# Performance work log

Measured on AMD Instinct MI355X. Metric: run time of the kernel, lower is better.

The kernel has to match this reference:

```python
import jax, jax.numpy as jnp
import numpy as np

# ---- static config (mirrors Anchors.__init__ defaults) ----
STRIDES = [8, 16, 32, 64]
SIZES = [32, 64, 128, 256]
RATIOS = np.array([0.5, 1.0, 2.0])
SCALES = np.array([2 ** 0, 2 ** (1.0 / 3.0), 2 ** (2.0 / 3.0)])
FG_IOU, BG_IOU = 0.5, 0.4
VAR_XY, VAR_WH = 0.1, 0.2


def _anchor_wh(box_size, ratios, scales):
    # Faithful to AnchorLayer.generate_anchors
    a = box_size * np.tile(scales, (2, len(ratios))).T  # [K, 2]
    areas = a[:, 0] * a[:, 1]
    rr = np.repeat(ratios, len(scales))
    w = np.sqrt(areas * rr)
    h = w / rr
    return np.stack([w, h], axis=1).astype(np.float32)  # [K, 2]


def _level_anchors(H, W, stride, box_size):
    wh = _anchor_wh(box_size, RATIOS, SCALES)            # [K, 2]
    K = wh.shape[0]
    xs = (np.arange(W, dtype=np.float32) + 0.5) * stride
    ys = (np.arange(H, dtype=np.float32) + 0.5) * stride
    gx, gy = np.meshgrid(xs, ys)                         # [H, W] each
    grid = np.stack([gx, gy], axis=-1)[:, :, None, :]    # [H, W, 1, 2]
    grid = np.broadcast_to(grid, (H, W, K, 2))
    whb = np.broadcast_to(wh[None, None], (H, W, K, 2))
    return np.concatenate([grid, whb], axis=-1).reshape(-1, 4)  # xywh


def make_anchors(feature_shapes):
    levels = [_level_anchors(h, w, s, bs)
              for (h, w), s, bs in zip(feature_shapes, STRIDES, SIZES)]
    anchors = jnp.asarray(np.concatenate(levels, axis=0))  # [A, 4] xywh
    half = anchors[:, 2:] * 0.5
    anchors_xyxy = jnp.concatenate([anchors[:, :2] - half,
                                    anchors[:, :2] + half], axis=-1)
    return anchors, anchors_xyxy


def batch_box_iou(a_xyxy, g_xyxy):
    # a_xyxy: [A, 4], g_xyxy: [B, M, 4] -> [B, A, M]
    lt = jnp.maximum(a_xyxy[None, :, None, :2], g_xyxy[:, None, :, :2])
    rb = jnp.minimum(a_xyxy[None, :, None, 2:], g_xyxy[:, None, :, 2:])
    wh = jnp.clip(rb - lt, 0.0)
    inter = wh[..., 0] * wh[..., 1]
    area_a = (a_xyxy[:, 2] - a_xyxy[:, 0]) * (a_xyxy[:, 3] - a_xyxy[:, 1])
    area_g = (g_xyxy[..., 2] - g_xyxy[..., 0]) * (g_xyxy[..., 3] - g_xyxy[..., 1])
    return inter / (area_a[None, :, None] + area_g[:, None, :] - inter)


def bbox_to_deltas(boxes_xyxy, anchors_xywh):
    # boxes_xyxy: [B, A, 4], anchors_xywh: [A, 4]
    axy, awh = anchors_xywh[:, :2], anchors_xywh[:, 2:]
    cxcy = (boxes_xyxy[..., :2] + boxes_xyxy[..., 2:]) * 0.5
    txy = (cxcy - axy) / (awh * VAR_XY)
    twh = jnp.log((boxes_xyxy[..., 2:] - boxes_xyxy[..., :2]) / awh) / VAR_WH
    return jnp.concatenate([txy, twh], axis=-1)


def setup_inputs() -> dict:
    key = jax.random.key(0)
    ks = jax.random.split(key, 8)
    B, M = 16, 64
    f3 = jax.random.normal(ks[0], (B, 64, 64, 64), dtype=jnp.float32)
    f4 = jax.random.normal(ks[1], (B, 64, 32, 32), dtype=jnp.float32)
    f5 = jax.random.normal(ks[2], (B, 64, 16, 16), dtype=jnp.float32)
    f6 = jax.random.normal(ks[3], (B, 64, 8, 8), dtype=jnp.float32)
    # valid gt boxes in a 512x512 image, xyxy format
    cxy = jax.random.uniform(ks[4], (B, M, 2), minval=60.0, maxval=452.0)
    wh = jax.random.uniform(ks[5], (B, M, 2), minval=10.0, maxval=110.0)
    gt_boxes = jnp.concatenate([cxy - wh * 0.5, cxy + wh * 0.5], axis=-1)
    gt_labels = jax.random.randint(ks[6], (B, M), 1, 21, dtype=jnp.int64)
    return {"f3": f3, "f4": f4, "f5": f5, "f6": f6,
            "gt_boxes": gt_boxes, "gt_labels": gt_labels}


def reference(f3, f4, f5, f6, gt_boxes, gt_labels):
    feats = [f3, f4, f5, f6]
    shapes = [f.shape[-2:] for f in feats]
    anchors, anchors_xyxy = make_anchors(shapes)      # [A,4], [A,4]

    ious = batch_box_iou(anchors_xyxy, gt_boxes)      # [B, A, M]
    best_iou = ious.max(axis=-1)                      # [B, A]
    best_idx = ious.argmax(axis=-1)                   # [B, A]

    mask_bg = best_iou < BG_IOU
    mask_ign = (best_iou > BG_IOU) & (best_iou < FG_IOU)

    labels = jnp.take_along_axis(gt_labels, best_idx, axis=1)     # [B, A]
    labels = jnp.where(mask_ign, -1, labels)
    labels = jnp.where(mask_bg, 0, labels)

    boxes = jnp.take_along_axis(gt_boxes, best_idx[..., None], axis=1)  # [B,A,4]
    loc_targets = bbox_to_deltas(boxes, anchors)      # [B, A, 4]
    cls_targets = labels                              # [B, A]
    return loc_targets, cls_targets
```

## Files before the change

### kernel.cpp

```cpp
#include <hip/hip_runtime.h>
#include <math.h>

#define A_TOTAL 48960
#define N_WAVES (A_TOTAL / 64)
#define M_GT    64
#define B_BATCH 16

__global__ __launch_bounds__(256) void prep_kernel(
    float4* __restrict__ rec, float4* __restrict__ rin, float4* __restrict__ win)
{
    const int a = blockIdx.x * 256 + threadIdx.x;
    if (a >= A_TOTAL) return;

    int local, W, stride, bs;
    if (a < 36864)      { local = a;         W = 64; stride = 8;  bs = 32;  }
    else if (a < 46080) { local = a - 36864; W = 32; stride = 16; bs = 64;  }
    else if (a < 48384) { local = a - 46080; W = 16; stride = 32; bs = 128; }
    else                { local = a - 48384; W = 8;  stride = 64; bs = 256; }

    const int hw = local / 9;
    const int k  = local - hw * 9;
    const int y  = hw / W;
    const int x  = hw - y * W;
    const int r  = k / 3;
    const int s  = k - r * 3;

    const double sc = (s == 0) ? 1.0 : ((s == 1) ? 1.2599210498948732
                                                 : 1.5874010519681994);
    const double rr = (r == 0) ? 0.5 : ((r == 1) ? 1.0 : 2.0);
    const double av   = (double)bs * sc;
    const double area = av * av;
    const double wd   = sqrt(area * rr);
    const double hd   = wd / rr;
    const float aw = (float)wd, ah = (float)hd;

    const float acx = ((float)x + 0.5f) * (float)stride;
    const float acy = ((float)y + 0.5f) * (float)stride;
    const float hx = aw * 0.5f, hy = ah * 0.5f;
    const float ax1 = acx - hx, ay1 = acy - hy;
    const float ax2 = acx + hx, ay2 = acy + hy;

    rec[a] = make_float4(acx, acy, aw, ah);
    rin[a] = make_float4(1.0f / (aw * 0.1f), 1.0f / (ah * 0.1f),
                         1.0f / aw,          1.0f / ah);

    float wx1 = ax1, wy1 = ay1, wx2 = ax2, wy2 = ay2;
    #pragma unroll
    for (int m = 1; m < 64; m <<= 1) {
        wx1 = fminf(wx1, __shfl_xor(wx1, m, 64));
        wy1 = fminf(wy1, __shfl_xor(wy1, m, 64));
        wx2 = fmaxf(wx2, __shfl_xor(wx2, m, 64));
        wy2 = fmaxf(wy2, __shfl_xor(wy2, m, 64));
    }
    if ((threadIdx.x & 63) == 0) win[a >> 6] = make_float4(wx1, wy1, wx2, wy2);
}

__global__ __launch_bounds__(256) void anchors_assign_kernel(
    const float*  __restrict__ gt_boxes,
    const int*    __restrict__ gt_labels,
    const float4* __restrict__ rec,
    const float4* __restrict__ rin,
    const float4* __restrict__ win,
    float* __restrict__ out_loc,
    float* __restrict__ out_cls)
{
    __shared__ float4 sbox[M_GT];
    __shared__ float  sarea[M_GT];
    __shared__ float  slab[M_GT];

    const int b   = blockIdx.y;
    const int tid = threadIdx.x;

    if (tid < M_GT) {
        float4 g = ((const float4*)gt_boxes)[b * M_GT + tid];
        sbox[tid]  = g;
        sarea[tid] = (g.z - g.x) * (g.w - g.y);
        slab[tid]  = (float)gt_labels[b * M_GT + tid];
    }
    __syncthreads();

    const int a = blockIdx.x * 256 + tid;
    if (a >= A_TOTAL) return;

    const float4 rc = rec[a];
    const float4 ri = rin[a];
    const float4 wv = win[a >> 6];

    const float acx = rc.x, acy = rc.y, aw = rc.z, ah = rc.w;
    const float hx = aw * 0.5f, hy = ah * 0.5f;
    const float ax1 = acx - hx, ay1 = acy - hy;
    const float ax2 = acx + hx, ay2 = acy + hy;
    const float areaA = (ax2 - ax1) * (ay2 - ay1);

    const int lane = tid & 63;
    const float4 gb = sbox[lane];
    const bool cand = (fminf(wv.z, gb.z) > fmaxf(wv.x, gb.x)) &&
                      (fminf(wv.w, gb.w) > fmaxf(wv.y, gb.y));
    unsigned long long mask = __ballot(cand);

    float b_inter = 0.0f, b_den = 1.0f;
    int   bidx = 0;
    while (mask) {
        const int j = (int)__builtin_ctzll(mask);
        mask &= mask - 1;
        const float4 g = sbox[j];
        const float ltx = fmaxf(ax1, g.x), lty = fmaxf(ay1, g.y);
        const float rbx = fminf(ax2, g.z), rby = fminf(ay2, g.w);
        const float wx = fmaxf(rbx - ltx, 0.0f);
        const float wy = fmaxf(rby - lty, 0.0f);
        const float inter = wx * wy;
        const float den   = (areaA + sarea[j]) - inter;
        if (inter * b_den > b_inter * den) {
            b_inter = inter; b_den = den; bidx = j;
        }
    }
    const float best = b_inter / b_den;

    float lab = slab[bidx];
    if (best > 0.4f && best < 0.5f) lab = -1.0f;
    if (best < 0.4f)                lab = 0.0f;

    const float4 g = sbox[bidx];
    const float gcx = (g.x + g.z) * 0.5f;
    const float gcy = (g.y + g.w) * 0.5f;
    const float tx = (gcx - acx) * ri.x;
    const float ty = (gcy - acy) * ri.y;
    const float tw = __logf((g.z - g.x) * ri.z) * 5.0f;
    const float th = __logf((g.w - g.y) * ri.w) * 5.0f;

    const size_t idx = (size_t)b * A_TOTAL + a;
    ((float4*)out_loc)[idx] = make_float4(tx, ty, tw, th);
    out_cls[idx] = lab;
}

extern "C" void kernel_launch(void* const* d_in, const int* in_sizes, int n_in,
                              void* d_out, int out_size, void* d_ws, size_t ws_size,
                              hipStream_t stream) {
    const float* gt_boxes  = (const float*)d_in[4];
    const int*   gt_labels = (const int*)d_in[5];

    float4* rec = (float4*)d_ws;
    float4* rin = rec + A_TOTAL;
    float4* win = rin + A_TOTAL;

    float* out_loc = (float*)d_out;
    float* out_cls = (float*)d_out + (size_t)B_BATCH * A_TOTAL * 4;

    prep_kernel<<<(A_TOTAL + 255) / 256, 256, 0, stream>>>(rec, rin, win);

    dim3 grid((A_TOTAL + 255) / 256, B_BATCH);
    anchors_assign_kernel<<<grid, 256, 0, stream>>>(gt_boxes, gt_labels,
                                                    rec, rin, win, out_loc, out_cls);
}
```

Before: 91.29 us.

## Process four batch images per block and software-pipeline candidate GT loads

```diff
diff --git a/kernel.cpp b/kernel.cpp
--- a/kernel.cpp
+++ b/kernel.cpp
@@ -5,6 +5,7 @@
 #define N_WAVES (A_TOTAL / 64)
 #define M_GT    64
 #define B_BATCH 16
+#define B_PER_BLK 4
 
 __global__ __launch_bounds__(256) void prep_kernel(
     float4* __restrict__ rec, float4* __restrict__ rin, float4* __restrict__ win)
@@ -64,18 +65,19 @@
     float* __restrict__ out_loc,
     float* __restrict__ out_cls)
 {
-    __shared__ float4 sbox[M_GT];
-    __shared__ float  sarea[M_GT];
-    __shared__ float  slab[M_GT];
+    __shared__ float4 sbox[B_PER_BLK][M_GT];
+    __shared__ float  sarea[B_PER_BLK][M_GT];
+    __shared__ float  slab[B_PER_BLK][M_GT];
 
-    const int b   = blockIdx.y;
+    const int b0  = blockIdx.y * B_PER_BLK;
     const int tid = threadIdx.x;
 
-    if (tid < M_GT) {
-        float4 g = ((const float4*)gt_boxes)[b * M_GT + tid];
-        sbox[tid]  = g;
-        sarea[tid] = (g.z - g.x) * (g.w - g.y);
-        slab[tid]  = (float)gt_labels[b * M_GT + tid];
+    {
+        const int bb = tid >> 6, j = tid & 63;
+        const float4 g = ((const float4*)gt_boxes)[(b0 + bb) * M_GT + j];
+        sbox[bb][j]  = g;
+        sarea[bb][j] = (g.z - g.x) * (g.w - g.y);
+        slab[bb][j]  = (float)gt_labels[(b0 + bb) * M_GT + j];
     }
     __syncthreads();
 
@@ -93,44 +95,60 @@
     const float areaA = (ax2 - ax1) * (ay2 - ay1);
 
     const int lane = tid & 63;
-    const float4 gb = sbox[lane];
-    const bool cand = (fminf(wv.z, gb.z) > fmaxf(wv.x, gb.x)) &&
-                      (fminf(wv.w, gb.w) > fmaxf(wv.y, gb.y));
-    unsigned long long mask = __ballot(cand);
 
-    float b_inter = 0.0f, b_den = 1.0f;
-    int   bidx = 0;
-    while (mask) {
-        const int j = (int)__builtin_ctzll(mask);
-        mask &= mask - 1;
-        const float4 g = sbox[j];
-        const float ltx = fmaxf(ax1, g.x), lty = fmaxf(ay1, g.y);
-        const float rbx = fminf(ax2, g.z), rby = fminf(ay2, g.w);
-        const float wx = fmaxf(rbx - ltx, 0.0f);
-        const float wy = fmaxf(rby - lty, 0.0f);
-        const float inter = wx * wy;
-        const float den   = (areaA + sarea[j]) - inter;
-        if (inter * b_den > b_inter * den) {
-            b_inter = inter; b_den = den; bidx = j;
+    #pragma unroll
+    for (int bb = 0; bb < B_PER_BLK; ++bb) {
+        const float4 gb = sbox[bb][lane];
+        const bool cand = (fminf(wv.z, gb.z) > fmaxf(wv.x, gb.x)) &&
+                          (fminf(wv.w, gb.w) > fmaxf(wv.y, gb.y));
+        unsigned long long mask = __ballot(cand);
+
+        float b_inter = 0.0f, b_den = 1.0f;
+        int   bidx = 0;
+        if (mask) {
+            int j = (int)__builtin_ctzll(mask);
+            mask &= mask - 1;
+            float4 g  = sbox[bb][j];
+            float  ga = sarea[bb][j];
+            while (true) {
+                int jn = -1; float4 gn; float gan = 0.0f;
+                if (mask) {
+                    jn = (int)__builtin_ctzll(mask);
+                    mask &= mask - 1;
+                    gn  = sbox[bb][jn];
+                    gan = sarea[bb][jn];
+                }
+                const float ltx = fmaxf(ax1, g.x), lty = fmaxf(ay1, g.y);
+                const float rbx = fminf(ax2, g.z), rby = fminf(ay2, g.w);
+                const float wx = fmaxf(rbx - ltx, 0.0f);
+                const float wy = fmaxf(rby - lty, 0.0f);
+                const float inter = wx * wy;
+                const float den   = (areaA + ga) - inter;
+                if (inter * b_den > b_inter * den) {
+                    b_inter = inter; b_den = den; bidx = j;
+                }
+                if (jn < 0) break;
+                j = jn; g = gn; ga = gan;
+            }
         }
+        const float best = b_inter / b_den;
+
+        float lab = slab[bb][bidx];
+        if (best > 0.4f && best < 0.5f) lab = -1.0f;
+        if (best < 0.4f)                lab = 0.0f;
+
+        const float4 g = sbox[bb][bidx];
+        const float gcx = (g.x + g.z) * 0.5f;
+        const float gcy = (g.y + g.w) * 0.5f;
+        const float tx = (gcx - acx) * ri.x;
+        const float ty = (gcy - acy) * ri.y;
+        const float tw = __logf((g.z - g.x) * ri.z) * 5.0f;
+        const float th = __logf((g.w - g.y) * ri.w) * 5.0f;
+
+        const size_t idx = (size_t)(b0 + bb) * A_TOTAL + a;
+        ((float4*)out_loc)[idx] = make_float4(tx, ty, tw, th);
+        out_cls[idx] = lab;
     }
-    const float best = b_inter / b_den;
-
-    float lab = slab[bidx];
-    if (best > 0.4f && best < 0.5f) lab = -1.0f;
-    if (best < 0.4f)                lab = 0.0f;
-
-    const float4 g = sbox[bidx];
-    const float gcx = (g.x + g.z) * 0.5f;
-    const float gcy = (g.y + g.w) * 0.5f;
-    const float tx = (gcx - acx) * ri.x;
-    const float ty = (gcy - acy) * ri.y;
-    const float tw = __logf((g.z - g.x) * ri.z) * 5.0f;
-    const float th = __logf((g.w - g.y) * ri.w) * 5.0f;
-
-    const size_t idx = (size_t)b * A_TOTAL + a;
-    ((float4*)out_loc)[idx] = make_float4(tx, ty, tw, th);
-    out_cls[idx] = lab;
 }
 
 extern "C" void kernel_launch(void* const* d_in, const int* in_sizes, int n_in,
@@ -148,7 +166,7 @@
 
     prep_kernel<<<(A_TOTAL + 255) / 256, 256, 0, stream>>>(rec, rin, win);
 
-    dim3 grid((A_TOTAL + 255) / 256, B_BATCH);
+    dim3 grid((A_TOTAL + 255) / 256, B_BATCH / B_PER_BLK);
     anchors_assign_kernel<<<grid, 256, 0, stream>>>(gt_boxes, gt_labels,
                                                     rec, rin, win, out_loc, out_cls);
 }
```

Measured after the change: 113.7 us. 24.5% more time.
